# Kernel optimization log

Measured on AMD Instinct MI355X. Metric: run time of the kernel, lower is better.

The kernel has to match this reference:

```python
import jax, jax.numpy as jnp
import numpy as np

B, H, N, D = 4, 16, 4096, 64
M = 256  # proj_len

def setup_inputs() -> dict:
    key = jax.random.key(0)
    k1, k2, k3, k4 = jax.random.split(key, 4)
    Q = jax.random.normal(k1, (B, H, N, D), dtype=jnp.float32)
    K = jax.random.normal(k2, (B, H, N, D), dtype=jnp.float32)
    V = jax.random.normal(k3, (B, H, N, D), dtype=jnp.float32)
    E = jax.random.normal(k4, (N, M), dtype=jnp.float32)
    return {"Q": Q, "K": K, "V": V, "E": E}

def reference(Q, K, V, E):
    # Low-rank sequence projection of K and V (shared E).
    K_proj = jnp.einsum('bhnd,nm->bhmd', K, E)  # [B,H,M,D]
    V_proj = jnp.einsum('bhnd,nm->bhmd', V, E)  # [B,H,M,D]
    # Standard scaled dot-product attention (flex_attention default score_mod).
    scale = 1.0 / jnp.sqrt(jnp.asarray(Q.shape[-1], Q.dtype))
    scores = jnp.einsum('bhnd,bhmd->bhnm', Q, K_proj) * scale  # [B,H,N,M]
    attn = jax.nn.softmax(scores, axis=-1)
    out = jnp.einsum('bhnm,bhmd->bhnd', attn, V_proj)  # [B,H,N,D]
    return out
```

## Files before the change

kernel.cpp:

```cpp
#include <hip/hip_runtime.h>

typedef __attribute__((ext_vector_type(8))) short bf16x8;
typedef __attribute__((ext_vector_type(8))) unsigned short u16x8;
typedef __attribute__((ext_vector_type(4))) float f32x4;

constexpr int BH  = 64;
constexpr int SEQ = 4096;
constexpr int DIM = 64;
constexpr int PM  = 256;
constexpr size_t PLANE = (size_t)BH * PM * DIM;

__device__ __forceinline__ unsigned short f2bf(float f){
    unsigned int u = __float_as_uint(f);
    return (unsigned short)((u + 0x7fffu + ((u >> 16) & 1u)) >> 16);
}
__device__ __forceinline__ float bf2f(unsigned short h){
    return __uint_as_float(((unsigned int)h) << 16);
}
__device__ __forceinline__ unsigned short f2h(float f){
    _Float16 h = (_Float16)f;
    unsigned short u;
    __builtin_memcpy(&u, &h, 2);
    return u;
}
__device__ __forceinline__ float h2f(unsigned short u){
    _Float16 h;
    __builtin_memcpy(&h, &u, 2);
    return (float)h;
}

__global__ __launch_bounds__(256) void prep_e_kernel(const float* __restrict__ E,
                                                     unsigned short* __restrict__ Et_hi,
                                                     unsigned short* __restrict__ Et_lo){
    __shared__ float T[64][65];
    int n0 = (blockIdx.x & 63) * 64;
    int m0 = (blockIdx.x >> 6) * 64;
    int t = threadIdx.x;
    #pragma unroll
    for (int i = 0; i < 16; ++i){
        int idx = t + i * 256;
        int nl = idx >> 6, ml = idx & 63;
        T[nl][ml] = E[(size_t)(n0 + nl) * PM + (m0 + ml)];
    }
    __syncthreads();
    #pragma unroll
    for (int i = 0; i < 16; ++i){
        int idx = t + i * 256;
        int ml = idx >> 6, nl = idx & 63;
        float v = T[nl][ml];
        unsigned short h = f2bf(v);
        unsigned short lo = f2bf(v - bf2f(h));
        size_t o = (size_t)(m0 + ml) * SEQ + (n0 + nl);
        Et_hi[o] = h;
        Et_lo[o] = lo;
    }
}

__global__ __launch_bounds__(256, 4) void proj_partial_kernel(const float* __restrict__ K,
                                                              const float* __restrict__ V,
                                                              const unsigned short* __restrict__ Et_hi,
                                                              const unsigned short* __restrict__ Et_lo,
                                                              unsigned short* __restrict__ PK,
                                                              unsigned short* __restrict__ PV){
    __shared__ unsigned short Kh[64][72], Kl[64][72], Vh[64][72];
    int bid   = blockIdx.x;
    int s     = bid & 7;
    int rest  = bid >> 3;
    int mh    = rest & 1;
    int bh    = rest >> 1;
    int nbase = s * (SEQ / 8);
    int t = threadIdx.x;
    int w = t >> 6, l = t & 63, l15 = l & 15, lg = l >> 4;
    int m0w = mh * 128 + w * 32;

    const float* Kb = K + (size_t)bh * SEQ * DIM;
    const float* Vb = V + (size_t)bh * SEQ * DIM;
    int d  = t & 63;
    int ng = t >> 6;

    f32x4 accK[2][4], accV[4][2];
    #pragma unroll
    for (int i = 0; i < 2; ++i)
        #pragma unroll
        for (int j = 0; j < 4; ++j){ accK[i][j] = (f32x4)0.0f; accV[j][i] = (f32x4)0.0f; }

    for (int n0 = nbase; n0 < nbase + SEQ / 8; n0 += 64){
        #pragma unroll
        for (int p = 0; p < 2; ++p){
            int nb = p * 32 + ng * 8;
            float kf[8], vf[8];
            #pragma unroll
            for (int i = 0; i < 8; ++i){
                kf[i] = Kb[(size_t)(n0 + nb + i) * DIM + d];
                vf[i] = Vb[(size_t)(n0 + nb + i) * DIM + d];
            }
            u16x8 kh, kl, vh;
            #pragma unroll
            for (int i = 0; i < 8; ++i){
                unsigned short h = f2bf(kf[i]);
                kh[i] = h;
                kl[i] = f2bf(kf[i] - bf2f(h));
                vh[i] = f2bf(vf[i]);
            }
            *reinterpret_cast<u16x8*>(&Kh[d][nb]) = kh;
            *reinterpret_cast<u16x8*>(&Kl[d][nb]) = kl;
            *reinterpret_cast<u16x8*>(&Vh[d][nb]) = vh;
        }
        __syncthreads();
        bf16x8 eh[2][2], el[2][2];
        #pragma unroll
        for (int nk = 0; nk < 2; ++nk){
            #pragma unroll
            for (int ms = 0; ms < 2; ++ms){
                size_t off = (size_t)(m0w + ms * 16 + l15) * SEQ + (n0 + nk * 32 + lg * 8);
                eh[nk][ms] = *reinterpret_cast<const bf16x8*>(Et_hi + off);
                el[nk][ms] = *reinterpret_cast<const bf16x8*>(Et_lo + off);
            }
        }
        #pragma unroll
        for (int nk = 0; nk < 2; ++nk){
            int kb = nk * 32 + lg * 8;
            #pragma unroll
            for (int dt = 0; dt < 4; ++dt){
                bf16x8 kh = *reinterpret_cast<const bf16x8*>(&Kh[dt * 16 + l15][kb]);
                bf16x8 kl = *reinterpret_cast<const bf16x8*>(&Kl[dt * 16 + l15][kb]);
                bf16x8 vh = *reinterpret_cast<const bf16x8*>(&Vh[dt * 16 + l15][kb]);
                #pragma unroll
                for (int ms = 0; ms < 2; ++ms){
                    accK[ms][dt] = __builtin_amdgcn_mfma_f32_16x16x32_bf16(eh[nk][ms], kh, accK[ms][dt], 0, 0, 0);
                    accK[ms][dt] = __builtin_amdgcn_mfma_f32_16x16x32_bf16(eh[nk][ms], kl, accK[ms][dt], 0, 0, 0);
                    accK[ms][dt] = __builtin_amdgcn_mfma_f32_16x16x32_bf16(el[nk][ms], kh, accK[ms][dt], 0, 0, 0);
                    accV[dt][ms] = __builtin_amdgcn_mfma_f32_16x16x32_bf16(vh, eh[nk][ms], accV[dt][ms], 0, 0, 0);
                }
            }
        }
        __syncthreads();
    }

    unsigned short* PKb = PK + ((size_t)s * BH + bh) * PM * DIM;
    unsigned short* PVb = PV + ((size_t)s * BH + bh) * DIM * PM;
    #pragma unroll
    for (int ms = 0; ms < 2; ++ms){
        #pragma unroll
        for (int dt = 0; dt < 4; ++dt){
            #pragma unroll
            for (int j = 0; j < 4; ++j){
                int mg = m0w + ms * 16 + lg * 4 + j;
                int dg = dt * 16 + l15;
                PKb[(size_t)mg * DIM + dg] = f2h(accK[ms][dt][j]);
                int dr = dt * 16 + lg * 4 + j;
                int mc = m0w + ms * 16 + l15;
                PVb[(size_t)dr * PM + mc] = f2h(accV[dt][ms][j]);
            }
        }
    }
}

__global__ __launch_bounds__(256) void reduce_kernel(const unsigned short* __restrict__ PK,
                                                     const unsigned short* __restrict__ PV,
                                                     unsigned short* __restrict__ Kp_hi,
                                                     unsigned short* __restrict__ Kp_lo,
                                                     unsigned short* __restrict__ Vpt){
    size_t e8 = (size_t)blockIdx.x * 256 + threadIdx.x;
    const u16x8* PK8 = reinterpret_cast<const u16x8*>(PK);
    const u16x8* PV8 = reinterpret_cast<const u16x8*>(PV);
    size_t stride8 = PLANE / 8;

    float k[8], v[8];
    {
        u16x8 a = PK8[e8];
        u16x8 b = PV8[e8];
        #pragma unroll
        for (int i = 0; i < 8; ++i){ k[i] = h2f(a[i]); v[i] = h2f(b[i]); }
    }
    #pragma unroll
    for (int s = 1; s < 8; ++s){
        u16x8 a = PK8[e8 + (size_t)s * stride8];
        u16x8 b = PV8[e8 + (size_t)s * stride8];
        #pragma unroll
        for (int i = 0; i < 8; ++i){ k[i] += h2f(a[i]); v[i] += h2f(b[i]); }
    }
    u16x8 hi, lo, vb;
    #pragma unroll
    for (int i = 0; i < 8; ++i){
        unsigned short h = f2bf(k[i]);
        hi[i] = h;
        lo[i] = f2bf(k[i] - bf2f(h));
        vb[i] = f2bf(v[i]);
    }
    *reinterpret_cast<u16x8*>(Kp_hi + e8 * 8) = hi;
    *reinterpret_cast<u16x8*>(Kp_lo + e8 * 8) = lo;
    *reinterpret_cast<u16x8*>(Vpt   + e8 * 8) = vb;
}

constexpr int ATTN_LDS_BYTES = (2 * 256 * 72 + 64 * 264 + 4 * 16 * 264) * 2;

__global__ __launch_bounds__(256, 1) void attn_kernel(const float* __restrict__ Q,
                                                      const unsigned short* __restrict__ Kp_hi,
                                                      const unsigned short* __restrict__ Kp_lo,
                                                      const unsigned short* __restrict__ Vpt,
                                                      float* __restrict__ Out){
    extern __shared__ unsigned short smem[];
    unsigned short (*Kh)[72]  = reinterpret_cast<unsigned short (*)[72]>(smem);
    unsigned short (*Kl)[72]  = reinterpret_cast<unsigned short (*)[72]>(smem + 256 * 72);
    unsigned short (*Vt)[264] = reinterpret_cast<unsigned short (*)[264]>(smem + 2 * 256 * 72);
    unsigned short* Pbase     = smem + 2 * 256 * 72 + 64 * 264;

    int bid  = blockIdx.x;
    int orig = (bid & 7) * 128 + (bid >> 3);
    int bh   = orig >> 4;
    int q0   = (orig & 15) * 256;
    int t = threadIdx.x;
    int w = t >> 6, l = t & 63, l15 = l & 15, lg = l >> 4;
    unsigned short (*Pw)[264] = reinterpret_cast<unsigned short (*)[264]>(Pbase + w * 16 * 264);

    const unsigned short* KHb = Kp_hi + (size_t)bh * PM * DIM;
    const unsigned short* KLb = Kp_lo + (size_t)bh * PM * DIM;
    const unsigned short* VTb = Vpt   + (size_t)bh * DIM * PM;
    #pragma unroll
    for (int i = 0; i < 8; ++i){
        int idx = i * 256 + t;
        int r = idx >> 3;
        int c = (idx & 7) * 8;
        u16x8 a = *reinterpret_cast<const u16x8*>(KHb + (size_t)idx * 8);
        u16x8 b = *reinterpret_cast<const u16x8*>(KLb + (size_t)idx * 8);
        *reinterpret_cast<u16x8*>(&Kh[r][c]) = a;
        *reinterpret_cast<u16x8*>(&Kl[r][c]) = b;
    }
    #pragma unroll
    for (int i = 0; i < 8; ++i){
        int idx = i * 256 + t;
        int r = idx >> 5;
        int c = (idx & 31) * 8;
        u16x8 a = *reinterpret_cast<const u16x8*>(VTb + (size_t)idx * 8);
        *reinterpret_cast<u16x8*>(&Vt[r][c]) = a;
    }
    __syncthreads();

    const float* Qw = Q   + ((size_t)bh * SEQ + q0 + w * 64) * DIM;
    float*       Ow = Out + ((size_t)bh * SEQ + q0 + w * 64) * DIM;

    for (int rt = 0; rt < 4; ++rt){
        bf16x8 qh[2], ql[2];
        {
            const float* Qb = Qw + (size_t)(rt * 16 + l15) * DIM;
            #pragma unroll
            for (int nk = 0; nk < 2; ++nk){
                float4 a = *reinterpret_cast<const float4*>(Qb + nk * 32 + lg * 8);
                float4 b = *reinterpret_cast<const float4*>(Qb + nk * 32 + lg * 8 + 4);
                float vals[8] = {a.x, a.y, a.z, a.w, b.x, b.y, b.z, b.w};
                #pragma unroll
                for (int i = 0; i < 8; ++i){
                    float v = vals[i] * 0.125f;
                    unsigned short h = f2bf(v);
                    qh[nk][i] = (short)h;
                    ql[nk][i] = (short)f2bf(v - bf2f(h));
                }
            }
        }

        f32x4 sa[16];
        #pragma unroll
        for (int i = 0; i < 16; ++i) sa[i] = (f32x4)0.0f;
        #pragma unroll
        for (int mi = 0; mi < 16; ++mi){
            #pragma unroll
            for (int nk = 0; nk < 2; ++nk){
                bf16x8 bh_ = *reinterpret_cast<const bf16x8*>(&Kh[mi * 16 + l15][nk * 32 + lg * 8]);
                bf16x8 bl_ = *reinterpret_cast<const bf16x8*>(&Kl[mi * 16 + l15][nk * 32 + lg * 8]);
                sa[mi] = __builtin_amdgcn_mfma_f32_16x16x32_bf16(qh[nk], bh_, sa[mi], 0, 0, 0);
                sa[mi] = __builtin_amdgcn_mfma_f32_16x16x32_bf16(qh[nk], bl_, sa[mi], 0, 0, 0);
                sa[mi] = __builtin_amdgcn_mfma_f32_16x16x32_bf16(ql[nk], bh_, sa[mi], 0, 0, 0);
            }
        }

        float inv[4];
        #pragma unroll
        for (int j = 0; j < 4; ++j){
            float mx = sa[0][j];
            #pragma unroll
            for (int mi = 1; mi < 16; ++mi) mx = fmaxf(mx, sa[mi][j]);
            #pragma unroll
            for (int o = 1; o < 16; o <<= 1) mx = fmaxf(mx, __shfl_xor(mx, o, 64));
            float sum = 0.0f;
            #pragma unroll
            for (int mi = 0; mi < 16; ++mi){
                float p = __expf(sa[mi][j] - mx);
                sa[mi][j] = p;
                sum += p;
            }
            #pragma unroll
            for (int o = 1; o < 16; o <<= 1) sum += __shfl_xor(sum, o, 64);
            inv[j] = 1.0f / sum;
        }

        #pragma unroll
        for (int mi = 0; mi < 16; ++mi){
            #pragma unroll
            for (int j = 0; j < 4; ++j){
                Pw[lg * 4 + j][mi * 16 + l15] = f2bf(sa[mi][j]);
            }
        }

        f32x4 oacc[4];
        #pragma unroll
        for (int i = 0; i < 4; ++i) oacc[i] = (f32x4)0.0f;
        #pragma unroll
        for (int mk = 0; mk < 8; ++mk){
            bf16x8 ap = *reinterpret_cast<const bf16x8*>(&Pw[l15][mk * 32 + lg * 8]);
            #pragma unroll
            for (int dt = 0; dt < 4; ++dt){
                bf16x8 bv = *reinterpret_cast<const bf16x8*>(&Vt[dt * 16 + l15][mk * 32 + lg * 8]);
                oacc[dt] = __builtin_amdgcn_mfma_f32_16x16x32_bf16(ap, bv, oacc[dt], 0, 0, 0);
            }
        }

        #pragma unroll
        for (int dt = 0; dt < 4; ++dt){
            #pragma unroll
            for (int j = 0; j < 4; ++j){
                Ow[(size_t)(rt * 16 + lg * 4 + j) * DIM + dt * 16 + l15] = oacc[dt][j] * inv[j];
            }
        }
    }
}

extern "C" void kernel_launch(void* const* d_in, const int* in_sizes, int n_in,
                              void* d_out, int out_size, void* d_ws, size_t ws_size,
                              hipStream_t stream){
    const float* Q = (const float*)d_in[0];
    const float* K = (const float*)d_in[1];
    const float* V = (const float*)d_in[2];
    const float* E = (const float*)d_in[3];
    float* out = (float*)d_out;

    unsigned short* Et_hi = (unsigned short*)d_ws;
    unsigned short* Et_lo = Et_hi + (size_t)PM * SEQ;
    unsigned short* Kp_hi = Et_lo + (size_t)PM * SEQ;
    unsigned short* Kp_lo = Kp_hi + PLANE;
    unsigned short* Vpt   = Kp_lo + PLANE;
    unsigned short* PK    = Vpt   + PLANE;
    unsigned short* PV    = PK    + 8 * PLANE;

    hipFuncSetAttribute(reinterpret_cast<const void*>(attn_kernel),
                        hipFuncAttributeMaxDynamicSharedMemorySize, ATTN_LDS_BYTES);

    prep_e_kernel<<<256, 256, 0, stream>>>(E, Et_hi, Et_lo);
    proj_partial_kernel<<<1024, 256, 0, stream>>>(K, V, Et_hi, Et_lo, PK, PV);
    reduce_kernel<<<PLANE / 8 / 256, 256, 0, stream>>>(PK, PV, Kp_hi, Kp_lo, Vpt);
    attn_kernel<<<1024, 256, ATTN_LDS_BYTES, stream>>>(Q, Kp_hi, Kp_lo, Vpt, out);
}
```

Before: 181.1 us.

## Split attention over two key halves with online softmax to double occupancy

The attention kernel now stages projected K/V in two halves of 128 and keeps a running max and sum (online softmax), which cuts LDS per block enough to launch two blocks per CU. Q is loaded once for all row tiles and the score MFMA operands are swapped, so P is written to LDS with packed 8-byte stores. Separately, the K projection partials are kept as fp32 instead of fp16, which adds memory traffic in the reduce step but avoids precision loss. The added state (four row tiles of output accumulators) raises register pressure, which may limit the intended occupancy gain.

```diff
diff --git a/kernel.cpp b/kernel.cpp
--- a/kernel.cpp
+++ b/kernel.cpp
@@ -60,7 +60,7 @@
                                                               const float* __restrict__ V,
                                                               const unsigned short* __restrict__ Et_hi,
                                                               const unsigned short* __restrict__ Et_lo,
-                                                              unsigned short* __restrict__ PK,
+                                                              float* __restrict__ PK,
                                                               unsigned short* __restrict__ PV){
     __shared__ unsigned short Kh[64][72], Kl[64][72], Vh[64][72];
     int bid   = blockIdx.x;
@@ -137,7 +137,7 @@
         __syncthreads();
     }
 
-    unsigned short* PKb = PK + ((size_t)s * BH + bh) * PM * DIM;
+    float*          PKb = PK + ((size_t)s * BH + bh) * PM * DIM;
     unsigned short* PVb = PV + ((size_t)s * BH + bh) * DIM * PM;
     #pragma unroll
     for (int ms = 0; ms < 2; ++ms){
@@ -147,7 +147,7 @@
             for (int j = 0; j < 4; ++j){
                 int mg = m0w + ms * 16 + lg * 4 + j;
                 int dg = dt * 16 + l15;
-                PKb[(size_t)mg * DIM + dg] = f2h(accK[ms][dt][j]);
+                PKb[(size_t)mg * DIM + dg] = accK[ms][dt][j];
                 int dr = dt * 16 + lg * 4 + j;
                 int mc = m0w + ms * 16 + l15;
                 PVb[(size_t)dr * PM + mc] = f2h(accV[dt][ms][j]);
@@ -156,29 +156,32 @@
     }
 }
 
-__global__ __launch_bounds__(256) void reduce_kernel(const unsigned short* __restrict__ PK,
+__global__ __launch_bounds__(256) void reduce_kernel(const float* __restrict__ PK,
                                                      const unsigned short* __restrict__ PV,
                                                      unsigned short* __restrict__ Kp_hi,
                                                      unsigned short* __restrict__ Kp_lo,
                                                      unsigned short* __restrict__ Vpt){
     size_t e8 = (size_t)blockIdx.x * 256 + threadIdx.x;
-    const u16x8* PK8 = reinterpret_cast<const u16x8*>(PK);
     const u16x8* PV8 = reinterpret_cast<const u16x8*>(PV);
     size_t stride8 = PLANE / 8;
 
     float k[8], v[8];
     {
-        u16x8 a = PK8[e8];
-        u16x8 b = PV8[e8];
-        #pragma unroll
-        for (int i = 0; i < 8; ++i){ k[i] = h2f(a[i]); v[i] = h2f(b[i]); }
+        float4 a = *reinterpret_cast<const float4*>(PK + e8 * 8);
+        float4 b = *reinterpret_cast<const float4*>(PK + e8 * 8 + 4);
+        k[0]=a.x; k[1]=a.y; k[2]=a.z; k[3]=a.w; k[4]=b.x; k[5]=b.y; k[6]=b.z; k[7]=b.w;
+        u16x8 c = PV8[e8];
+        #pragma unroll
+        for (int i = 0; i < 8; ++i) v[i] = h2f(c[i]);
     }
     #pragma unroll
     for (int s = 1; s < 8; ++s){
-        u16x8 a = PK8[e8 + (size_t)s * stride8];
-        u16x8 b = PV8[e8 + (size_t)s * stride8];
-        #pragma unroll
-        for (int i = 0; i < 8; ++i){ k[i] += h2f(a[i]); v[i] += h2f(b[i]); }
+        float4 a = *reinterpret_cast<const float4*>(PK + (size_t)s * PLANE + e8 * 8);
+        float4 b = *reinterpret_cast<const float4*>(PK + (size_t)s * PLANE + e8 * 8 + 4);
+        k[0]+=a.x; k[1]+=a.y; k[2]+=a.z; k[3]+=a.w; k[4]+=b.x; k[5]+=b.y; k[6]+=b.z; k[7]+=b.w;
+        u16x8 c = PV8[e8 + (size_t)s * stride8];
+        #pragma unroll
+        for (int i = 0; i < 8; ++i) v[i] += h2f(c[i]);
     }
     u16x8 hi, lo, vb;
     #pragma unroll
@@ -193,18 +196,18 @@
     *reinterpret_cast<u16x8*>(Vpt   + e8 * 8) = vb;
 }
 
-constexpr int ATTN_LDS_BYTES = (2 * 256 * 72 + 64 * 264 + 4 * 16 * 264) * 2;
-
-__global__ __launch_bounds__(256, 1) void attn_kernel(const float* __restrict__ Q,
+constexpr int ATTN_LDS_BYTES = (2 * 128 * 72 + 64 * 136 + 4 * 16 * 136) * 2;
+
+__global__ __launch_bounds__(256, 2) void attn_kernel(const float* __restrict__ Q,
                                                       const unsigned short* __restrict__ Kp_hi,
                                                       const unsigned short* __restrict__ Kp_lo,
                                                       const unsigned short* __restrict__ Vpt,
                                                       float* __restrict__ Out){
     extern __shared__ unsigned short smem[];
     unsigned short (*Kh)[72]  = reinterpret_cast<unsigned short (*)[72]>(smem);
-    unsigned short (*Kl)[72]  = reinterpret_cast<unsigned short (*)[72]>(smem + 256 * 72);
-    unsigned short (*Vt)[264] = reinterpret_cast<unsigned short (*)[264]>(smem + 2 * 256 * 72);
-    unsigned short* Pbase     = smem + 2 * 256 * 72 + 64 * 264;
+    unsigned short (*Kl)[72]  = reinterpret_cast<unsigned short (*)[72]>(smem + 128 * 72);
+    unsigned short (*Vt)[136] = reinterpret_cast<unsigned short (*)[136]>(smem + 2 * 128 * 72);
+    unsigned short* Pbase     = smem + 2 * 128 * 72 + 64 * 136;
 
     int bid  = blockIdx.x;
     int orig = (bid & 7) * 128 + (bid >> 3);
@@ -212,116 +215,136 @@
     int q0   = (orig & 15) * 256;
     int t = threadIdx.x;
     int w = t >> 6, l = t & 63, l15 = l & 15, lg = l >> 4;
-    unsigned short (*Pw)[264] = reinterpret_cast<unsigned short (*)[264]>(Pbase + w * 16 * 264);
+    unsigned short (*Pw)[136] = reinterpret_cast<unsigned short (*)[136]>(Pbase + w * 16 * 136);
+
+    const float* Qw = Q   + ((size_t)bh * SEQ + q0 + w * 64) * DIM;
+    float*       Ow = Out + ((size_t)bh * SEQ + q0 + w * 64) * DIM;
+
+    bf16x8 qh[4][2], ql[4][2];
+    #pragma unroll
+    for (int rt = 0; rt < 4; ++rt){
+        const float* Qb = Qw + (size_t)(rt * 16 + l15) * DIM;
+        #pragma unroll
+        for (int nk = 0; nk < 2; ++nk){
+            float4 a = *reinterpret_cast<const float4*>(Qb + nk * 32 + lg * 8);
+            float4 b = *reinterpret_cast<const float4*>(Qb + nk * 32 + lg * 8 + 4);
+            float vals[8] = {a.x, a.y, a.z, a.w, b.x, b.y, b.z, b.w};
+            #pragma unroll
+            for (int i = 0; i < 8; ++i){
+                float v = vals[i] * 0.125f;
+                unsigned short h = f2bf(v);
+                qh[rt][nk][i] = (short)h;
+                ql[rt][nk][i] = (short)f2bf(v - bf2f(h));
+            }
+        }
+    }
 
     const unsigned short* KHb = Kp_hi + (size_t)bh * PM * DIM;
     const unsigned short* KLb = Kp_lo + (size_t)bh * PM * DIM;
     const unsigned short* VTb = Vpt   + (size_t)bh * DIM * PM;
-    #pragma unroll
-    for (int i = 0; i < 8; ++i){
-        int idx = i * 256 + t;
-        int r = idx >> 3;
-        int c = (idx & 7) * 8;
-        u16x8 a = *reinterpret_cast<const u16x8*>(KHb + (size_t)idx * 8);
-        u16x8 b = *reinterpret_cast<const u16x8*>(KLb + (size_t)idx * 8);
-        *reinterpret_cast<u16x8*>(&Kh[r][c]) = a;
-        *reinterpret_cast<u16x8*>(&Kl[r][c]) = b;
-    }
-    #pragma unroll
-    for (int i = 0; i < 8; ++i){
-        int idx = i * 256 + t;
-        int r = idx >> 5;
-        int c = (idx & 31) * 8;
-        u16x8 a = *reinterpret_cast<const u16x8*>(VTb + (size_t)idx * 8);
-        *reinterpret_cast<u16x8*>(&Vt[r][c]) = a;
-    }
-    __syncthreads();
-
-    const float* Qw = Q   + ((size_t)bh * SEQ + q0 + w * 64) * DIM;
-    float*       Ow = Out + ((size_t)bh * SEQ + q0 + w * 64) * DIM;
-
+
+    float mx[4], sm[4];
+    f32x4 oacc[4][4];
+    #pragma unroll
     for (int rt = 0; rt < 4; ++rt){
-        bf16x8 qh[2], ql[2];
-        {
-            const float* Qb = Qw + (size_t)(rt * 16 + l15) * DIM;
-            #pragma unroll
-            for (int nk = 0; nk < 2; ++nk){
-                float4 a = *reinterpret_cast<const float4*>(Qb + nk * 32 + lg * 8);
-                float4 b = *reinterpret_cast<const float4*>(Qb + nk * 32 + lg * 8 + 4);
-                float vals[8] = {a.x, a.y, a.z, a.w, b.x, b.y, b.z, b.w};
-                #pragma unroll
-                for (int i = 0; i < 8; ++i){
-                    float v = vals[i] * 0.125f;
-                    unsigned short h = f2bf(v);
-                    qh[nk][i] = (short)h;
-                    ql[nk][i] = (short)f2bf(v - bf2f(h));
+        mx[rt] = -3.0e38f; sm[rt] = 0.0f;
+        #pragma unroll
+        for (int dt = 0; dt < 4; ++dt) oacc[rt][dt] = (f32x4)0.0f;
+    }
+
+    #pragma unroll
+    for (int h = 0; h < 2; ++h){
+        if (h) __syncthreads();
+        #pragma unroll
+        for (int i = 0; i < 4; ++i){
+            int idx = i * 256 + t;
+            int r = idx >> 3, c = (idx & 7) * 8;
+            *reinterpret_cast<u16x8*>(&Kh[r][c]) = *reinterpret_cast<const u16x8*>(KHb + (size_t)(h * 128 + r) * DIM + c);
+            *reinterpret_cast<u16x8*>(&Kl[r][c]) = *reinterpret_cast<const u16x8*>(KLb + (size_t)(h * 128 + r) * DIM + c);
+        }
+        #pragma unroll
+        for (int i = 0; i < 4; ++i){
+            int idx = i * 256 + t;
+            int r = idx >> 4, c = (idx & 15) * 8;
+            *reinterpret_cast<u16x8*>(&Vt[r][c]) = *reinterpret_cast<const u16x8*>(VTb + (size_t)r * PM + h * 128 + c);
+        }
+        __syncthreads();
+
+        #pragma unroll
+        for (int rt = 0; rt < 4; ++rt){
+            f32x4 sa[8];
+            #pragma unroll
+            for (int i = 0; i < 8; ++i) sa[i] = (f32x4)0.0f;
+            #pragma unroll
+            for (int mi = 0; mi < 8; ++mi){
+                #pragma unroll
+                for (int nk = 0; nk < 2; ++nk){
+                    bf16x8 kh_ = *reinterpret_cast<const bf16x8*>(&Kh[mi * 16 + l15][nk * 32 + lg * 8]);
+                    bf16x8 kl_ = *reinterpret_cast<const bf16x8*>(&Kl[mi * 16 + l15][nk * 32 + lg * 8]);
+                    sa[mi] = __builtin_amdgcn_mfma_f32_16x16x32_bf16(kh_, qh[rt][nk], sa[mi], 0, 0, 0);
+                    sa[mi] = __builtin_amdgcn_mfma_f32_16x16x32_bf16(kl_, qh[rt][nk], sa[mi], 0, 0, 0);
+                    sa[mi] = __builtin_amdgcn_mfma_f32_16x16x32_bf16(kh_, ql[rt][nk], sa[mi], 0, 0, 0);
                 }
             }
-        }
-
-        f32x4 sa[16];
-        #pragma unroll
-        for (int i = 0; i < 16; ++i) sa[i] = (f32x4)0.0f;
-        #pragma unroll
-        for (int mi = 0; mi < 16; ++mi){
-            #pragma unroll
-            for (int nk = 0; nk < 2; ++nk){
-                bf16x8 bh_ = *reinterpret_cast<const bf16x8*>(&Kh[mi * 16 + l15][nk * 32 + lg * 8]);
-                bf16x8 bl_ = *reinterpret_cast<const bf16x8*>(&Kl[mi * 16 + l15][nk * 32 + lg * 8]);
-                sa[mi] = __builtin_amdgcn_mfma_f32_16x16x32_bf16(qh[nk], bh_, sa[mi], 0, 0, 0);
-                sa[mi] = __builtin_amdgcn_mfma_f32_16x16x32_bf16(qh[nk], bl_, sa[mi], 0, 0, 0);
-                sa[mi] = __builtin_amdgcn_mfma_f32_16x16x32_bf16(ql[nk], bh_, sa[mi], 0, 0, 0);
-            }
-        }
-
-        float inv[4];
-        #pragma unroll
-        for (int j = 0; j < 4; ++j){
-            float mx = sa[0][j];
-            #pragma unroll
-            for (int mi = 1; mi < 16; ++mi) mx = fmaxf(mx, sa[mi][j]);
-            #pragma unroll
-            for (int o = 1; o < 16; o <<= 1) mx = fmaxf(mx, __shfl_xor(mx, o, 64));
-            float sum = 0.0f;
-            #pragma unroll
-            for (int mi = 0; mi < 16; ++mi){
-                float p = __expf(sa[mi][j] - mx);
-                sa[mi][j] = p;
-                sum += p;
-            }
-            #pragma unroll
-            for (int o = 1; o < 16; o <<= 1) sum += __shfl_xor(sum, o, 64);
-            inv[j] = 1.0f / sum;
-        }
-
-        #pragma unroll
-        for (int mi = 0; mi < 16; ++mi){
-            #pragma unroll
-            for (int j = 0; j < 4; ++j){
-                Pw[lg * 4 + j][mi * 16 + l15] = f2bf(sa[mi][j]);
-            }
-        }
-
-        f32x4 oacc[4];
-        #pragma unroll
-        for (int i = 0; i < 4; ++i) oacc[i] = (f32x4)0.0f;
-        #pragma unroll
-        for (int mk = 0; mk < 8; ++mk){
-            bf16x8 ap = *reinterpret_cast<const bf16x8*>(&Pw[l15][mk * 32 + lg * 8]);
-            #pragma unroll
-            for (int dt = 0; dt < 4; ++dt){
-                bf16x8 bv = *reinterpret_cast<const bf16x8*>(&Vt[dt * 16 + l15][mk * 32 + lg * 8]);
-                oacc[dt] = __builtin_amdgcn_mfma_f32_16x16x32_bf16(ap, bv, oacc[dt], 0, 0, 0);
-            }
-        }
-
-        #pragma unroll
-        for (int dt = 0; dt < 4; ++dt){
-            #pragma unroll
-            for (int j = 0; j < 4; ++j){
-                Ow[(size_t)(rt * 16 + lg * 4 + j) * DIM + dt * 16 + l15] = oacc[dt][j] * inv[j];
-            }
-        }
+            float hm = -3.0e38f;
+            #pragma unroll
+            for (int mi = 0; mi < 8; ++mi)
+                #pragma unroll
+                for (int j = 0; j < 4; ++j) hm = fmaxf(hm, sa[mi][j]);
+            hm = fmaxf(hm, __shfl_xor(hm, 16, 64));
+            hm = fmaxf(hm, __shfl_xor(hm, 32, 64));
+            float nm = fmaxf(mx[rt], hm);
+            float sc = __expf(mx[rt] - nm);
+            mx[rt] = nm;
+            float ps = 0.0f;
+            #pragma unroll
+            for (int mi = 0; mi < 8; ++mi)
+                #pragma unroll
+                for (int j = 0; j < 4; ++j){
+                    float p = __expf(sa[mi][j] - nm);
+                    sa[mi][j] = p;
+                    ps += p;
+                }
+            ps += __shfl_xor(ps, 16, 64);
+            ps += __shfl_xor(ps, 32, 64);
+            sm[rt] = sm[rt] * sc + ps;
+            #pragma unroll
+            for (int mi = 0; mi < 8; ++mi){
+                unsigned int d0 = (unsigned int)f2bf(sa[mi][0]) | ((unsigned int)f2bf(sa[mi][1]) << 16);
+                unsigned int d1 = (unsigned int)f2bf(sa[mi][2]) | ((unsigned int)f2bf(sa[mi][3]) << 16);
+                uint2 dd; dd.x = d0; dd.y = d1;
+                *reinterpret_cast<uint2*>(&Pw[l15][mi * 16 + lg * 4]) = dd;
+            }
+            float scj[4];
+            #pragma unroll
+            for (int j = 0; j < 4; ++j) scj[j] = __shfl(sc, lg * 20 + j, 64);
+            #pragma unroll
+            for (int dt = 0; dt < 4; ++dt)
+                #pragma unroll
+                for (int j = 0; j < 4; ++j) oacc[rt][dt][j] *= scj[j];
+            #pragma unroll
+            for (int mk = 0; mk < 4; ++mk){
+                bf16x8 ap = *reinterpret_cast<const bf16x8*>(&Pw[l15][mk * 32 + lg * 8]);
+                #pragma unroll
+                for (int dt = 0; dt < 4; ++dt){
+                    bf16x8 bv = *reinterpret_cast<const bf16x8*>(&Vt[dt * 16 + l15][mk * 32 + lg * 8]);
+                    oacc[rt][dt] = __builtin_amdgcn_mfma_f32_16x16x32_bf16(ap, bv, oacc[rt][dt], 0, 0, 0);
+                }
+            }
+        }
+    }
+
+    #pragma unroll
+    for (int rt = 0; rt < 4; ++rt){
+        float inv = 1.0f / sm[rt];
+        float invj[4];
+        #pragma unroll
+        for (int j = 0; j < 4; ++j) invj[j] = __shfl(inv, lg * 20 + j, 64);
+        #pragma unroll
+        for (int dt = 0; dt < 4; ++dt)
+            #pragma unroll
+            for (int j = 0; j < 4; ++j)
+                Ow[(size_t)(rt * 16 + lg * 4 + j) * DIM + dt * 16 + l15] = oacc[rt][dt][j] * invj[j];
     }
 }
 
@@ -339,8 +362,9 @@
     unsigned short* Kp_hi = Et_lo + (size_t)PM * SEQ;
     unsigned short* Kp_lo = Kp_hi + PLANE;
     unsigned short* Vpt   = Kp_lo + PLANE;
-    unsigned short* PK    = Vpt   + PLANE;
-    unsigned short* PV    = PK    + 8 * PLANE;
+    size_t base_bytes = ((size_t)PM * SEQ * 2 + PLANE * 3) * sizeof(unsigned short);
+    float* PK          = reinterpret_cast<float*>((char*)d_ws + base_bytes);
+    unsigned short* PV = reinterpret_cast<unsigned short*>(PK + 8 * PLANE);
 
     hipFuncSetAttribute(reinterpret_cast<const void*>(attn_kernel),
                         hipFuncAttributeMaxDynamicSharedMemorySize, ATTN_LDS_BYTES);
```

After: 163.2 us. -9.9%, faster.
